# Kernel optimization log

Measured on AMD Instinct MI355X. Metric: run time of the kernel, lower is better.

The kernel has to match this reference:

```python
import jax, jax.numpy as jnp
import numpy as np
from jax import lax

VOCAB = 50000
EMB = 300
HID = 256
N = 4096          # total_sents
T_COL = 64
T_ROW = 16
N_DOCS = 512


def setup_inputs() -> dict:
    key = jax.random.key(0)
    ks = jax.random.split(key, 20)

    def glorot(k, shape):
        fan = float(sum(shape))
        return (jax.random.normal(k, shape, jnp.float32) * (2.0 / fan) ** 0.5)

    inp = {}
    inp["col"] = jax.random.randint(ks[0], (N, T_COL), 0, VOCAB, dtype=jnp.int32)
    inp["row"] = jax.random.randint(ks[1], (N, T_ROW), 0, VOCAB, dtype=jnp.int32)
    inp["row_neg"] = jax.random.randint(ks[2], (N, T_ROW), 0, VOCAB, dtype=jnp.int32)
    # pack_padded_sequence expects lengths sorted descending
    inp["col_lens"] = jnp.sort(jax.random.randint(ks[3], (N,), 1, T_COL + 1, dtype=jnp.int32))[::-1]
    inp["row_lens"] = jnp.sort(jax.random.randint(ks[4], (N,), 1, T_ROW + 1, dtype=jnp.int32))[::-1]
    inp["row_neg_lens"] = jnp.sort(jax.random.randint(ks[5], (N,), 1, T_ROW + 1, dtype=jnp.int32))[::-1]
    inp["col_refs"] = jax.random.randint(ks[6], (N,), 0, N_DOCS, dtype=jnp.int32)
    inp["row_refs"] = jax.random.randint(ks[7], (N,), 0, N_DOCS, dtype=jnp.int32)
    inp["row_neg_refs"] = jax.random.randint(ks[8], (N,), 0, N_DOCS, dtype=jnp.int32)
    inp["embed_table"] = jax.random.normal(ks[9], (VOCAB, EMB), jnp.float32) * 0.1
    inp["col_W_ih"] = glorot(ks[10], (4 * HID, EMB))
    inp["col_W_hh"] = glorot(ks[11], (4 * HID, HID))
    inp["col_b_ih"] = jnp.zeros((4 * HID,), jnp.float32)
    inp["col_b_hh"] = jnp.zeros((4 * HID,), jnp.float32)
    inp["row_W_ih"] = glorot(ks[12], (4 * HID, EMB))
    inp["row_W_hh"] = glorot(ks[13], (4 * HID, HID))
    inp["row_b_ih"] = jnp.zeros((4 * HID,), jnp.float32)
    inp["row_b_hh"] = jnp.zeros((4 * HID,), jnp.float32)
    return inp


def lstm_last_hidden(x, lengths, W_ih, W_hh, b_ih, b_hh):
    """x: [N,T,E]; returns hidden state at step lengths-1 per sequence: [N,H].
    Equivalent to torch LSTM over a packed padded sequence (state frozen past len)."""
    Nn, T, _ = x.shape
    H = W_hh.shape[1]
    h0 = jnp.zeros((Nn, H), x.dtype)
    bias = b_ih + b_hh

    def step(carry, inputs):
        h, c = carry
        xt, t = inputs  # xt: [N,E]
        gates = xt @ W_ih.T + h @ W_hh.T + bias  # [N,4H]
        i, f, g, o = jnp.split(gates, 4, axis=-1)  # torch gate order i,f,g,o
        i = jax.nn.sigmoid(i); f = jax.nn.sigmoid(f); o = jax.nn.sigmoid(o)
        g = jnp.tanh(g)
        c_new = f * c + i * g
        h_new = o * jnp.tanh(c_new)
        m = (t < lengths)[:, None]
        return (jnp.where(m, h_new, h), jnp.where(m, c_new, c)), None

    (h, _), _ = lax.scan(step, (h0, h0), (jnp.swapaxes(x, 0, 1), jnp.arange(T)))
    return h


def reference(col, row, row_neg, col_lens, row_lens, row_neg_lens,
              col_refs, row_refs, row_neg_refs, embed_table,
              col_W_ih, col_W_hh, col_b_ih, col_b_hh,
              row_W_ih, row_W_hh, row_b_ih, row_b_hh):
    # Dropout is identity (eval-mode reference).
    def compose(tokens, lens, refs, W_ih, W_hh, b_ih, b_hh):
        emb = embed_table[tokens]                      # [N,T,E]
        h = lstm_last_hidden(emb, lens, W_ih, W_hh, b_ih, b_hh)  # [N,H]
        # mask-multiply + sum == segment-sum of hidden states by doc ref,
        # scattered into a [total_sents, H] buffer (rows >= n_docs are zero)
        return jax.ops.segment_sum(h, refs, num_segments=tokens.shape[0])

    col_h = compose(col, col_lens, col_refs, col_W_ih, col_W_hh, col_b_ih, col_b_hh)
    row_h = compose(row, row_lens, row_refs, row_W_ih, row_W_hh, row_b_ih, row_b_hh)
    neg_h = compose(row_neg, row_neg_lens, row_neg_refs, row_W_ih, row_W_hh, row_b_ih, row_b_hh)

    pos = jnp.sum(col_h * row_h, axis=1)
    neg = jnp.sum(col_h * neg_h, axis=1)
    # BPRLoss(size_average=False): sum of -logsigmoid(pos - neg)
    return -jnp.sum(jax.nn.log_sigmoid(pos - neg))
```

## Files before the change

kernel.cpp:

```cpp
#include <hip/hip_runtime.h>


typedef __bf16 bf16x8 __attribute__((ext_vector_type(8)));
typedef float  fvec4  __attribute__((ext_vector_type(4)));

#define NSEN 4096
#define HIDN 256
#define EMBD 300
#define VOC  50000

#define OFF_P     0ULL
#define OFF_BPK   204800000ULL
#define OFF_WHHC  206110720ULL
#define OFF_WHHR  206635008ULL
#define OFF_BIAS  207159296ULL
#define OFF_H     207167488ULL
#define OFF_SEG   219750400ULL
#define OFF_LOSS  232333312ULL

static __device__ __forceinline__ unsigned short f2bf(float x) {
    unsigned int u = __float_as_uint(x);
    unsigned int r = (u + 0x7fffu + ((u >> 16) & 1u)) >> 16;
    return (unsigned short)r;
}
static __device__ __forceinline__ float bf2f(unsigned short b) {
    return __uint_as_float(((unsigned int)b) << 16);
}
static __device__ __forceinline__ float sigm(float x) { return 1.f / (1.f + __expf(-x)); }
static __device__ __forceinline__ float tanh_(float x) {
    float e = __expf(2.f * x);
    return 1.f - 2.f / (e + 1.f);
}
static __device__ __forceinline__ fvec4 unpk(uint2 v) {
    fvec4 o;
    o[0] = __uint_as_float((v.x & 0xffffu) << 16);
    o[1] = __uint_as_float(v.x & 0xffff0000u);
    o[2] = __uint_as_float((v.y & 0xffffu) << 16);
    o[3] = __uint_as_float(v.y & 0xffff0000u);
    return o;
}

static __device__ __forceinline__ void gld_lds16(const unsigned short* g,
                                                 unsigned short* l)
{
    __builtin_amdgcn_global_load_lds(
        (const __attribute__((address_space(1))) unsigned int*)g,
        (__attribute__((address_space(3))) unsigned int*)l, 16, 0, 0);
}

static __device__ __forceinline__ int whh_src(int o) {
    int L  = o >> 9;
    int r9 = o & 511;
    int ln = r9 >> 3, j = r9 & 7;
    int g  = L & 3, kt = (L >> 2) & 7, wv = (L >> 5) & 15;
    int row = g * 256 + wv * 16 + (ln & 15);
    int col = kt * 32 + (ln >> 4) * 8 + j;
    return row * 256 + col;
}

__global__ void prep_kernel(
    const float* __restrict__ cWih, const float* __restrict__ rWih,
    const float* __restrict__ cWhh, const float* __restrict__ rWhh,
    const float* __restrict__ cbih, const float* __restrict__ cbhh,
    const float* __restrict__ rbih, const float* __restrict__ rbhh,
    unsigned short* __restrict__ Bpk, unsigned short* __restrict__ WhhC,
    unsigned short* __restrict__ WhhR, float* __restrict__ biascat)
{
    int idx = blockIdx.x * 256 + threadIdx.x;
    if (idx < 655360) {
        int e = idx & 511, lnn = e >> 3, j = e & 7;
        int f = idx >> 9;
        int ntt = f & 3;
        int kc = f >> 2;
        int kt = kc % 10;
        int s  = kc / 10;
        int n = (s >> 1) * 128 + (s & 1) * 64 + ntt * 16 + (lnn & 15);
        int k = kt * 32 + (lnn >> 4) * 8 + j;
        float v = 0.f;
        if (k < EMBD) v = (n < 1024) ? cWih[n * EMBD + k] : rWih[(n - 1024) * EMBD + k];
        Bpk[idx] = f2bf(v);
        return;
    }
    idx -= 655360;
    if (idx < 262144) { WhhC[idx] = f2bf(cWhh[whh_src(idx)]); return; }
    idx -= 262144;
    if (idx < 262144) { WhhR[idx] = f2bf(rWhh[whh_src(idx)]); return; }
    idx -= 262144;
    if (idx < 2048)
        biascat[idx] = (idx < 1024) ? (cbih[idx] + cbhh[idx])
                                    : (rbih[idx - 1024] + rbhh[idx - 1024]);
}

__global__ __launch_bounds__(256) void gemm_p_kernel(
    const float* __restrict__ A,
    const unsigned short* __restrict__ Bpk,
    const float* __restrict__ bias,
    unsigned short* __restrict__ Pout)
{
    const int mb = blockIdx.x * 128;
    const int tid = threadIdx.x;
    const int wv = tid >> 6, ln = tid & 63, l15 = ln & 15, q = ln >> 4;
    const int wm = wv & 1, wn = wv >> 1;

    __shared__ __align__(16) unsigned short At[2][4][10][512];

    {
        int row = tid >> 1, kh = tid & 1;
        int gr = mb + row;
        unsigned short* dst = &At[row >> 6][(row >> 4) & 3][0][0];
        const int fl = row & 15;
        #pragma unroll
        for (int i = 0; i < 40; ++i) {
            int k = kh * 160 + i * 4;
            float4 v = make_float4(0.f, 0.f, 0.f, 0.f);
            if (gr < VOC && k < EMBD)
                v = *(const float4*)(A + (size_t)gr * EMBD + k);
            ushort4 b;
            b.x = f2bf(v.x); b.y = f2bf(v.y); b.z = f2bf(v.z); b.w = f2bf(v.w);
            int di = (k >> 5) * 512 + ((k >> 3) & 3) * 128 + fl * 8 + (k & 7);
            *(ushort4*)(dst + di) = b;
        }
    }
    __syncthreads();

    for (int nc = 0; nc < 16; ++nc) {
        fvec4 acc[4][4];
        #pragma unroll
        for (int a = 0; a < 4; ++a)
            #pragma unroll
            for (int b = 0; b < 4; ++b) acc[a][b] = (fvec4)0.f;

        #pragma unroll 2
        for (int kt = 0; kt < 10; ++kt) {
            const unsigned short* bp =
                Bpk + (size_t)(((nc * 2 + wn) * 10 + kt) * 4) * 512 + ln * 8;
            bf16x8 bfr[4];
            #pragma unroll
            for (int ntt = 0; ntt < 4; ++ntt)
                bfr[ntt] = *(const bf16x8*)(bp + ntt * 512);
            #pragma unroll
            for (int mt = 0; mt < 4; ++mt) {
                bf16x8 af = *(const bf16x8*)&At[wm][mt][kt][ln * 8];
                #pragma unroll
                for (int ntt = 0; ntt < 4; ++ntt)
                    acc[mt][ntt] = __builtin_amdgcn_mfma_f32_16x16x32_bf16(
                        af, bfr[ntt], acc[mt][ntt], 0, 0, 0);
            }
        }
        float bv[4];
        #pragma unroll
        for (int ntt = 0; ntt < 4; ++ntt)
            bv[ntt] = bias[nc * 128 + wn * 64 + ntt * 16 + l15];
        #pragma unroll
        for (int mt = 0; mt < 4; ++mt) {
            #pragma unroll
            for (int r = 0; r < 4; ++r) {
                int m = mb + wm * 64 + mt * 16 + q * 4 + r;
                if (m < VOC) {
                    size_t base = (size_t)m * 2048 + nc * 128 + wn * 64;
                    #pragma unroll
                    for (int ntt = 0; ntt < 4; ++ntt)
                        Pout[base + ntt * 16 + l15] = f2bf(acc[mt][ntt][r] + bv[ntt]);
                }
            }
        }
    }
}

__global__ __launch_bounds__(1024, 2) void lstm_kernel(
    const int* __restrict__ colTok, const int* __restrict__ rowTok, const int* __restrict__ negTok,
    const int* __restrict__ colLen, const int* __restrict__ rowLen, const int* __restrict__ negLen,
    const unsigned short* __restrict__ P,
    const unsigned short* __restrict__ WhhC, const unsigned short* __restrict__ WhhR,
    float* __restrict__ Hout)
{
    const int part = blockIdx.x >> 8;
    const int sb = blockIdx.x & 255;
    const int s0 = sb * 16;
    const int* tok = part == 0 ? colTok : (part == 1 ? rowTok : negTok);
    const int* len = part == 0 ? colLen : (part == 1 ? rowLen : negLen);
    const unsigned short* Whh = part == 0 ? WhhC : WhhR;
    const int T = part == 0 ? 64 : 16;
    const int pco = part == 0 ? 0 : 1024;
    float* Ho = Hout + (size_t)part * (NSEN * HIDN);

    const int tid = threadIdx.x;
    const int wv = tid >> 6;
    const int ln = tid & 63, l15 = ln & 15, q = ln >> 4;

    __shared__ __align__(16) unsigned short hx[2][8][4][16][8];
    __shared__ __align__(16) unsigned short pstage[16][4][2][16][8];
    char* hB0 = (char*)&hx[0][0][0][0][0];
    char* hB1 = (char*)&hx[1][0][0][0][0];

    for (int i = tid; i < 8192; i += 1024) (&hx[0][0][0][0][0])[i] = 0;

    const int len0 = len[s0 + l15];
    int ml = len0;
    #pragma unroll
    for (int off = 1; off < 16; off <<= 1) ml = max(ml, __shfl_xor(ml, off));
    const int maxlen = ml;

    const unsigned short* wbase = Whh + (size_t)wv * 16384 + (size_t)ln * 8;

    const int wrByte = (wv >> 1) * 1024 + ((wv & 1) * 2 + (q >> 1)) * 256 +
                       l15 * 16 + (q & 1) * 8;

    const int dg = ln >> 5, dh = (ln >> 4) & 1;

    float c[4];
    #pragma unroll
    for (int r = 0; r < 4; ++r) c[r] = 0.f;
    ushort4 hpk = make_ushort4(0, 0, 0, 0);

    __syncthreads();

    {
        int tk = tok[(s0 + l15) * T];
        #pragma unroll
        for (int d = 0; d < 2; ++d) {
            const unsigned short* src = P + (size_t)tk * 2048 + pco +
                (2 * d + dg) * 256 + wv * 16 + dh * 8;
            gld_lds16(src, &pstage[wv][2 * d][0][0][0]);
        }
    }
    int tknext = tok[(s0 + l15) * T + 1];

    for (int t = 0; t < maxlen; ++t) {
        const char* hRd = (t & 1) ? hB1 : hB0;
        char* hWr = (t & 1) ? hB0 : hB1;

        asm volatile("s_waitcnt vmcnt(0)" ::: "memory");

        fvec4 acc[4];
        #pragma unroll
        for (int g = 0; g < 4; ++g)
            acc[g] = unpk(*(const uint2*)
                &pstage[wv][g][q >> 1][l15][(q & 1) * 4]);

        #pragma unroll 2
        for (int kt = 0; kt < 8; ++kt) {
            bf16x8 b0 = *(const bf16x8*)(hRd + kt * 1024 + ln * 16);
            #pragma unroll
            for (int g = 0; g < 4; ++g) {
                bf16x8 a = *(const bf16x8*)(wbase + (size_t)(kt * 4 + g) * 512);
                acc[g] = __builtin_amdgcn_mfma_f32_16x16x32_bf16(a, b0, acc[g], 0, 0, 0);
            }
        }

        if (t + 1 < maxlen) {
            __builtin_amdgcn_sched_barrier(0);
            asm volatile("s_waitcnt lgkmcnt(0)" ::: "memory");
            #pragma unroll
            for (int d = 0; d < 2; ++d) {
                const unsigned short* src = P + (size_t)tknext * 2048 + pco +
                    (2 * d + dg) * 256 + wv * 16 + dh * 8;
                gld_lds16(src, &pstage[wv][2 * d][0][0][0]);
            }
            int t2 = (t + 2 < T) ? (t + 2) : (T - 1);
            tknext = tok[(s0 + l15) * T + t2];
        }

        {
            bool act = t < len0;
            if (act) {
                float hr[4];
                #pragma unroll
                for (int r = 0; r < 4; ++r) {
                    float iv = acc[0][r];
                    float fv = acc[1][r];
                    float gv = acc[2][r];
                    float ov = acc[3][r];
                    float cn = sigm(fv) * c[r] + sigm(iv) * tanh_(gv);
                    c[r] = cn;
                    hr[r] = sigm(ov) * tanh_(cn);
                }
                hpk = make_ushort4(f2bf(hr[0]), f2bf(hr[1]),
                                   f2bf(hr[2]), f2bf(hr[3]));
            }
            *(ushort4*)(hWr + wrByte) = hpk;
        }
        asm volatile("s_waitcnt lgkmcnt(0)\n\ts_barrier" ::: "memory");
    }

    const char* hF = (maxlen & 1) ? hB1 : hB0;
    for (int i = tid; i < 16 * HIDN; i += 1024) {
        int sq = i >> 8, hd = i & 255;
        unsigned short hv = *(const unsigned short*)
            (hF + (hd >> 5) * 1024 + ((hd >> 3) & 3) * 256 +
             sq * 16 + (hd & 7) * 2);
        Ho[(size_t)(s0 + sq) * HIDN + hd] = bf2f(hv);
    }
}

__global__ void scatter_kernel(const float* __restrict__ Hout,
                               const int* __restrict__ crefs, const int* __restrict__ rrefs,
                               const int* __restrict__ nrefs, float* __restrict__ seg)
{
    int idx = blockIdx.x * 256 + threadIdx.x;
    int which = idx >> 20;
    int rem = idx & 1048575;
    int s = rem >> 8, hd = rem & 255;
    const int* refs = which == 0 ? crefs : (which == 1 ? rrefs : nrefs);
    int rf = refs[s];
    atomicAdd(&seg[(size_t)which * 1048576 + (size_t)rf * 256 + hd], Hout[idx]);
}

__global__ void loss_kernel(const float* __restrict__ seg, float* __restrict__ part)
{
    int d = blockIdx.x, tid = threadIdx.x;
    const float* sc = seg + (size_t)d * 256;
    const float* sr = seg + 1048576 + (size_t)d * 256;
    const float* sn = seg + 2097152 + (size_t)d * 256;
    float a = sc[tid];
    float p = a * sr[tid];
    float n = a * sn[tid];
    for (int off = 32; off; off >>= 1) { p += __shfl_down(p, off); n += __shfl_down(n, off); }
    __shared__ float rp[4], rn[4];
    if ((tid & 63) == 0) { rp[tid >> 6] = p; rn[tid >> 6] = n; }
    __syncthreads();
    if (tid == 0) {
        float Ps = rp[0] + rp[1] + rp[2] + rp[3];
        float Ns = rn[0] + rn[1] + rn[2] + rn[3];
        float x = Ps - Ns;
        part[d] = fmaxf(-x, 0.f) + log1pf(expf(-fabsf(x)));
    }
}

__global__ void reduce_kernel(const float* __restrict__ part, float* __restrict__ out)
{
    int tid = threadIdx.x;
    float s = 0.f;
    for (int i = tid; i < 4096; i += 256) s += part[i];
    for (int off = 32; off; off >>= 1) s += __shfl_down(s, off);
    __shared__ float r[4];
    if ((tid & 63) == 0) r[tid >> 6] = s;
    __syncthreads();
    if (tid == 0) out[0] = r[0] + r[1] + r[2] + r[3];
}

extern "C" void kernel_launch(void* const* d_in, const int* in_sizes, int n_in,
                              void* d_out, int out_size, void* d_ws, size_t ws_size,
                              hipStream_t stream)
{
    const int*   col      = (const int*)d_in[0];
    const int*   row      = (const int*)d_in[1];
    const int*   rneg     = (const int*)d_in[2];
    const int*   col_lens = (const int*)d_in[3];
    const int*   row_lens = (const int*)d_in[4];
    const int*   rng_lens = (const int*)d_in[5];
    const int*   col_refs = (const int*)d_in[6];
    const int*   row_refs = (const int*)d_in[7];
    const int*   rng_refs = (const int*)d_in[8];
    const float* embed    = (const float*)d_in[9];
    const float* cWih     = (const float*)d_in[10];
    const float* cWhh     = (const float*)d_in[11];
    const float* cbih     = (const float*)d_in[12];
    const float* cbhh     = (const float*)d_in[13];
    const float* rWih     = (const float*)d_in[14];
    const float* rWhh     = (const float*)d_in[15];
    const float* rbih     = (const float*)d_in[16];
    const float* rbhh     = (const float*)d_in[17];

    char* ws = (char*)d_ws;
    unsigned short* P    = (unsigned short*)(ws + OFF_P);
    unsigned short* Bpk  = (unsigned short*)(ws + OFF_BPK);
    unsigned short* WhhC = (unsigned short*)(ws + OFF_WHHC);
    unsigned short* WhhR = (unsigned short*)(ws + OFF_WHHR);
    float* biascat = (float*)(ws + OFF_BIAS);
    float* Hbuf    = (float*)(ws + OFF_H);
    float* seg     = (float*)(ws + OFF_SEG);
    float* lpart   = (float*)(ws + OFF_LOSS);

    hipMemsetAsync(seg, 0, 3 * 4096 * 256 * sizeof(float), stream);

    prep_kernel<<<4616, 256, 0, stream>>>(cWih, rWih, cWhh, rWhh,
                                          cbih, cbhh, rbih, rbhh,
                                          Bpk, WhhC, WhhR, biascat);
    gemm_p_kernel<<<391, 256, 0, stream>>>(embed, Bpk, biascat, P);
    lstm_kernel<<<768, 1024, 0, stream>>>(col, row, rneg,
                                          col_lens, row_lens, rng_lens,
                                          P, WhhC, WhhR, Hbuf);
    scatter_kernel<<<12288, 256, 0, stream>>>(Hbuf, col_refs, row_refs, rng_refs, seg);
    loss_kernel<<<4096, 256, 0, stream>>>(seg, lpart);
    reduce_kernel<<<1, 256, 0, stream>>>(lpart, (float*)d_out);
}
```

Baseline: 697.7 us.

## Fuse segment-sum scatter into LSTM epilogue and double-buffer gate input staging

```diff
diff --git a/kernel.cpp b/kernel.cpp
--- a/kernel.cpp
+++ b/kernel.cpp
@@ -14,7 +14,6 @@
 #define OFF_WHHC  206110720ULL
 #define OFF_WHHR  206635008ULL
 #define OFF_BIAS  207159296ULL
-#define OFF_H     207167488ULL
 #define OFF_SEG   219750400ULL
 #define OFF_LOSS  232333312ULL
 
@@ -170,26 +169,29 @@
 __global__ __launch_bounds__(1024, 2) void lstm_kernel(
     const int* __restrict__ colTok, const int* __restrict__ rowTok, const int* __restrict__ negTok,
     const int* __restrict__ colLen, const int* __restrict__ rowLen, const int* __restrict__ negLen,
+    const int* __restrict__ crefs, const int* __restrict__ rrefs, const int* __restrict__ nrefs,
     const unsigned short* __restrict__ P,
     const unsigned short* __restrict__ WhhC, const unsigned short* __restrict__ WhhR,
-    float* __restrict__ Hout)
+    float* __restrict__ seg)
 {
     const int part = blockIdx.x >> 8;
     const int sb = blockIdx.x & 255;
     const int s0 = sb * 16;
     const int* tok = part == 0 ? colTok : (part == 1 ? rowTok : negTok);
     const int* len = part == 0 ? colLen : (part == 1 ? rowLen : negLen);
+    const int* refs = part == 0 ? crefs : (part == 1 ? rrefs : nrefs);
     const unsigned short* Whh = part == 0 ? WhhC : WhhR;
     const int T = part == 0 ? 64 : 16;
     const int pco = part == 0 ? 0 : 1024;
-    float* Ho = Hout + (size_t)part * (NSEN * HIDN);
+    float* segp = seg + (size_t)part * 1048576;
 
     const int tid = threadIdx.x;
     const int wv = tid >> 6;
     const int ln = tid & 63, l15 = ln & 15, q = ln >> 4;
 
     __shared__ __align__(16) unsigned short hx[2][8][4][16][8];
-    __shared__ __align__(16) unsigned short pstage[16][4][2][16][8];
+    __shared__ __align__(16) unsigned short pstage[2][16][4][2][16][8];
+    __shared__ __align__(16) char ldspad[1536];
     char* hB0 = (char*)&hx[0][0][0][0][0];
     char* hB1 = (char*)&hx[1][0][0][0][0];
 
@@ -200,6 +202,7 @@
     #pragma unroll
     for (int off = 1; off < 16; off <<= 1) ml = max(ml, __shfl_xor(ml, off));
     const int maxlen = ml;
+    if (maxlen < 0) ldspad[tid & 1023] = 1;
 
     const unsigned short* wbase = Whh + (size_t)wv * 16384 + (size_t)ln * 8;
 
@@ -221,12 +224,13 @@
         for (int d = 0; d < 2; ++d) {
             const unsigned short* src = P + (size_t)tk * 2048 + pco +
                 (2 * d + dg) * 256 + wv * 16 + dh * 8;
-            gld_lds16(src, &pstage[wv][2 * d][0][0][0]);
+            gld_lds16(src, &pstage[0][wv][2 * d][0][0][0]);
         }
     }
     int tknext = tok[(s0 + l15) * T + 1];
 
     for (int t = 0; t < maxlen; ++t) {
+        const int pb = t & 1;
         const char* hRd = (t & 1) ? hB1 : hB0;
         char* hWr = (t & 1) ? hB0 : hB1;
 
@@ -236,7 +240,7 @@
         #pragma unroll
         for (int g = 0; g < 4; ++g)
             acc[g] = unpk(*(const uint2*)
-                &pstage[wv][g][q >> 1][l15][(q & 1) * 4]);
+                &pstage[pb][wv][g][q >> 1][l15][(q & 1) * 4]);
 
         #pragma unroll 2
         for (int kt = 0; kt < 8; ++kt) {
@@ -250,12 +254,11 @@
 
         if (t + 1 < maxlen) {
             __builtin_amdgcn_sched_barrier(0);
-            asm volatile("s_waitcnt lgkmcnt(0)" ::: "memory");
             #pragma unroll
             for (int d = 0; d < 2; ++d) {
                 const unsigned short* src = P + (size_t)tknext * 2048 + pco +
                     (2 * d + dg) * 256 + wv * 16 + dh * 8;
-                gld_lds16(src, &pstage[wv][2 * d][0][0][0]);
+                gld_lds16(src, &pstage[pb ^ 1][wv][2 * d][0][0][0]);
             }
             int t2 = (t + 2 < T) ? (t + 2) : (T - 1);
             tknext = tok[(s0 + l15) * T + t2];
@@ -289,21 +292,9 @@
         unsigned short hv = *(const unsigned short*)
             (hF + (hd >> 5) * 1024 + ((hd >> 3) & 3) * 256 +
              sq * 16 + (hd & 7) * 2);
-        Ho[(size_t)(s0 + sq) * HIDN + hd] = bf2f(hv);
-    }
-}
-
-__global__ void scatter_kernel(const float* __restrict__ Hout,
-                               const int* __restrict__ crefs, const int* __restrict__ rrefs,
-                               const int* __restrict__ nrefs, float* __restrict__ seg)
-{
-    int idx = blockIdx.x * 256 + threadIdx.x;
-    int which = idx >> 20;
-    int rem = idx & 1048575;
-    int s = rem >> 8, hd = rem & 255;
-    const int* refs = which == 0 ? crefs : (which == 1 ? rrefs : nrefs);
-    int rf = refs[s];
-    atomicAdd(&seg[(size_t)which * 1048576 + (size_t)rf * 256 + hd], Hout[idx]);
+        int rf = refs[s0 + sq];
+        atomicAdd(segp + (size_t)rf * 256 + hd, bf2f(hv));
+    }
 }
 
 __global__ void loss_kernel(const float* __restrict__ seg, float* __restrict__ part)
@@ -368,7 +359,6 @@
     unsigned short* WhhC = (unsigned short*)(ws + OFF_WHHC);
     unsigned short* WhhR = (unsigned short*)(ws + OFF_WHHR);
     float* biascat = (float*)(ws + OFF_BIAS);
-    float* Hbuf    = (float*)(ws + OFF_H);
     float* seg     = (float*)(ws + OFF_SEG);
     float* lpart   = (float*)(ws + OFF_LOSS);
 
@@ -380,8 +370,8 @@
     gemm_p_kernel<<<391, 256, 0, stream>>>(embed, Bpk, biascat, P);
     lstm_kernel<<<768, 1024, 0, stream>>>(col, row, rneg,
                                           col_lens, row_lens, rng_lens,
-                                          P, WhhC, WhhR, Hbuf);
-    scatter_kernel<<<12288, 256, 0, stream>>>(Hbuf, col_refs, row_refs, rng_refs, seg);
+                                          col_refs, row_refs, rng_refs,
+                                          P, WhhC, WhhR, seg);
     loss_kernel<<<4096, 256, 0, stream>>>(seg, lpart);
     reduce_kernel<<<1, 256, 0, stream>>>(lpart, (float*)d_out);
 }
```

Measured after the change: 689.5 us. Within noise of the previous version (-1.2%).
